# Kernel tuning notes

Hardware: AMD Instinct MI355X
Metric: run time of the kernel (lower is better)

The kernel has to match this reference:

```python
import jax, jax.numpy as jnp
import numpy as np

N_HEADS = 8
DIM = 128
BT, A, M = 2880, 10, 350  # bs*T, agents, map tokens (from forwards())
TOPK_SELF, TOPK_CROSS = 3, 32


def _split_heads(x, h):
    B, T, C = x.shape
    return x.reshape(B, T, h, C // h).transpose(0, 2, 1, 3)  # [B,h,T,hd]


def _biased_attn(q, k, v, pe, rel):
    """flex_attention with score_mod: score + pe[b,q,rel[b,q,kv],h], -inf where rel==-1.
    q:[B,H,Tq,d] k,v:[B,H,Tk,d] pe:[B,Tq,K,H] rel:[B,Tq,Tk] int"""
    d = q.shape[-1]
    scores = jnp.einsum('bhqd,bhkd->bhqk', q, k) / jnp.sqrt(jnp.asarray(d, q.dtype))
    safe = jnp.maximum(rel, 0)
    bias = jnp.take_along_axis(pe, safe[:, :, :, None], axis=2)  # [B,Tq,Tk,H]
    bias = bias.transpose(0, 3, 1, 2)                            # [B,H,Tq,Tk]
    scores = jnp.where(rel[:, None, :, :] > -1, scores + bias, -jnp.inf)
    attn = jax.nn.softmax(scores, axis=-1)
    out = jnp.einsum('bhqk,bhkd->bhqd', attn, v)
    B, H, Tq, hd = out.shape
    return out.transpose(0, 2, 1, 3).reshape(B, Tq, H * hd)


def _make_relation(key, B, Tq, Tk, topk):
    # topk random keys per query get offsets 0..topk-1 in ascending kv order; rest -1
    rand = jax.random.uniform(key, (B, Tq, Tk))
    idx = jnp.sort(jax.lax.top_k(rand, topk)[1], axis=-1)  # [B,Tq,topk]
    rel = jnp.full((B, Tq, Tk), -1, dtype=jnp.int32)
    b = jnp.arange(B)[:, None, None]
    qi = jnp.arange(Tq)[None, :, None]
    return rel.at[b, qi, idx].set(jnp.arange(topk, dtype=jnp.int32)[None, None, :])


def setup_inputs() -> dict:
    key = jax.random.key(0)
    ks = jax.random.split(key, 12)
    s = 0.02
    return {
        'a_token': jax.random.normal(ks[0], (BT, A, DIM), jnp.float32),
        'm_token': jax.random.normal(ks[1], (BT, M, DIM), jnp.float32),
        'a2m_pe': jax.random.uniform(ks[2], (BT, A, TOPK_CROSS, N_HEADS), jnp.float32),
        'a_pe': jax.random.uniform(ks[3], (BT, A, TOPK_SELF, N_HEADS), jnp.float32),
        'Wq': s * jax.random.normal(ks[4], (DIM, DIM), jnp.float32),
        'Wk': s * jax.random.normal(ks[5], (DIM, DIM), jnp.float32),
        'Wv': s * jax.random.normal(ks[6], (DIM, DIM), jnp.float32),
        'W_cross_proj': s * jax.random.normal(ks[7], (DIM, DIM), jnp.float32),
        'W_cattn': s * jax.random.normal(ks[8], (DIM, 3 * DIM), jnp.float32),
        'W_self_proj': s * jax.random.normal(ks[9], (DIM, DIM), jnp.float32),
        'a2m_relation': _make_relation(ks[10], BT, A, M, TOPK_CROSS),
        'a_relation': _make_relation(ks[11], BT, A, A, TOPK_SELF),
    }


def reference(a_token, m_token, a2m_pe, a_pe, Wq, Wk, Wv, W_cross_proj,
              W_cattn, W_self_proj, a2m_relation, a_relation):
    # cross attention: q from a_token, k/v from m_token (dropout=0 => identity)
    q = _split_heads(a_token @ Wq, N_HEADS)
    k = _split_heads(m_token @ Wk, N_HEADS)
    v = _split_heads(m_token @ Wv, N_HEADS)
    y = _biased_attn(q, k, v, a2m_pe, a2m_relation) @ W_cross_proj
    # self attention with fused qkv projection
    q2, k2, v2 = jnp.split(y @ W_cattn, 3, axis=-1)
    y2 = _biased_attn(_split_heads(q2, N_HEADS), _split_heads(k2, N_HEADS),
                      _split_heads(v2, N_HEADS), a_pe, a_relation)
    return y2 @ W_self_proj
```

## Files before the change

### kernel.cpp

```cpp
#include <hip/hip_runtime.h>
#include <hip/hip_bf16.h>


typedef __attribute__((ext_vector_type(4))) float f32x4;
typedef __attribute__((ext_vector_type(8))) short bf16x8v;
typedef __attribute__((ext_vector_type(4))) short short4v;

#define BT_N 2880
#define A_N  10
#define M_N  350
#define BQ_N (BT_N * A_N)
#define DIMC 128

static __device__ __forceinline__ short f2b(float x) {
    __hip_bfloat16 b = __float2bfloat16(x);
    return __builtin_bit_cast(short, b);
}
static __device__ __forceinline__ float b2f(short s) {
    unsigned u = ((unsigned)(unsigned short)s) << 16;
    return __builtin_bit_cast(float, u);
}

__global__ __launch_bounds__(256) void precompute_mats(
    const float* __restrict__ Wq, const float* __restrict__ Wk,
    const float* __restrict__ Wv, const float* __restrict__ Wcp,
    const float* __restrict__ Wc, const float* __restrict__ Wsp,
    short* __restrict__ S1t, short* __restrict__ VP1t,
    short* __restrict__ S2t, short* __restrict__ VP2t)
{
    int gid = blockIdx.x * 256 + threadIdx.x;
    int mat = gid >> 17;
    int idx = gid & 131071;
    float acc = 0.f;
    if (mat == 0) {
        int n = idx >> 7, c = idx & 127;
        int h = n >> 7, d = n & 127;
        #pragma unroll
        for (int t = 0; t < 16; ++t)
            acc += Wq[c * 128 + h * 16 + t] * Wk[d * 128 + h * 16 + t];
        S1t[idx] = f2b(acc * 0.25f);
    } else if (mat == 1) {
        int d = idx >> 10, o = idx & 1023;
        int h = o >> 7, c = o & 127;
        #pragma unroll
        for (int t = 0; t < 16; ++t)
            acc += Wv[c * 128 + h * 16 + t] * Wcp[(h * 16 + t) * 128 + d];
        VP1t[idx] = f2b(acc);
    } else if (mat == 2) {
        int n = idx >> 7, c = idx & 127;
        int h = n >> 7, d = n & 127;
        #pragma unroll
        for (int t = 0; t < 16; ++t)
            acc += Wc[c * 384 + h * 16 + t] * Wc[d * 384 + 128 + h * 16 + t];
        S2t[idx] = f2b(acc * 0.25f);
    } else {
        int d = idx >> 10, o = idx & 1023;
        int h = o >> 7, c = o & 127;
        #pragma unroll
        for (int t = 0; t < 16; ++t)
            acc += Wc[c * 384 + 256 + h * 16 + t] * Wsp[(h * 16 + t) * 128 + d];
        VP2t[idx] = f2b(acc);
    }
}

__global__ __launch_bounds__(256) void conv_bf16(
    const float* __restrict__ in, short* __restrict__ out)
{
    int i = blockIdx.x * 256 + threadIdx.x;
    f32x4 a = ((const f32x4*)in)[2 * i];
    f32x4 b = ((const f32x4*)in)[2 * i + 1];
    bf16x8v t;
    t[0] = f2b(a.x); t[1] = f2b(a.y); t[2] = f2b(a.z); t[3] = f2b(a.w);
    t[4] = f2b(b.x); t[5] = f2b(b.y); t[6] = f2b(b.z); t[7] = f2b(b.w);
    ((bf16x8v*)out)[i] = t;
}

template<bool CF32>
__global__ __launch_bounds__(256) void gemm_bt(
    const short* __restrict__ Ap, const short* __restrict__ Bt,
    void* __restrict__ Cp, int M, int N, int K)
{
    __shared__ short As[128][72];
    __shared__ short Bs[128][72];
    const int tid  = threadIdx.x;
    const int bm   = blockIdx.y << 7, bn = blockIdx.x << 7;
    const int wave = tid >> 6, lane = tid & 63;
    const int wm   = (wave >> 1) << 6, wn = (wave & 1) << 6;
    const int row16 = lane & 15, kq = (lane >> 4) << 3;
    f32x4 acc[4][4] = {};

    for (int k0 = 0; k0 < K; k0 += 64) {
        #pragma unroll
        for (int i = 0; i < 4; ++i) {
            int g = (i << 8) + tid;
            int r = g >> 3, c = (g & 7) << 3;
            *(bf16x8v*)&As[r][c] = *(const bf16x8v*)(Ap + (size_t)(bm + r) * K + k0 + c);
        }
        #pragma unroll
        for (int i = 0; i < 4; ++i) {
            int g = (i << 8) + tid;
            int r = g >> 3, c = (g & 7) << 3;
            *(bf16x8v*)&Bs[r][c] = *(const bf16x8v*)(Bt + (size_t)(bn + r) * K + k0 + c);
        }
        __syncthreads();
        #pragma unroll
        for (int kk = 0; kk < 64; kk += 32) {
            bf16x8v afr[4], bfr[4];
            #pragma unroll
            for (int mi = 0; mi < 4; ++mi)
                afr[mi] = *(const bf16x8v*)&As[wm + (mi << 4) + row16][kq + kk];
            #pragma unroll
            for (int ni = 0; ni < 4; ++ni)
                bfr[ni] = *(const bf16x8v*)&Bs[wn + (ni << 4) + row16][kq + kk];
            #pragma unroll
            for (int mi = 0; mi < 4; ++mi)
                #pragma unroll
                for (int ni = 0; ni < 4; ++ni)
                    acc[mi][ni] = __builtin_amdgcn_mfma_f32_16x16x32_bf16(
                        afr[mi], bfr[ni], acc[mi][ni], 0, 0, 0);
        }
        __syncthreads();
    }

    const int col = lane & 15, rb = (lane >> 4) << 2;
    #pragma unroll
    for (int mi = 0; mi < 4; ++mi)
        #pragma unroll
        for (int ni = 0; ni < 4; ++ni)
            #pragma unroll
            for (int r = 0; r < 4; ++r) {
                int rr = bm + wm + (mi << 4) + rb + r;
                int cc = bn + wn + (ni << 4) + col;
                float v = acc[mi][ni][r];
                if (CF32) ((float*)Cp)[(size_t)rr * N + cc] = v;
                else      ((short*)Cp)[(size_t)rr * N + cc] = f2b(v);
            }
}

__global__ __launch_bounds__(256) void attn_cross(
    const float* __restrict__ m_token, const short* __restrict__ qS,
    const float* __restrict__ pe, const int* __restrict__ rel,
    short* __restrict__ u)
{
    __shared__ short mrows[32][136];
    __shared__ short qsr[16][136];
    __shared__ float sc[32][17];
    __shared__ float wts[8][33];
    __shared__ float peL[256];
    __shared__ int   selk[32];

    const int phys = blockIdx.x;
    const int b    = (phys & 7) * 360 + (phys >> 3) / A_N;
    const int q    = (phys >> 3) % A_N;
    const int bq   = b * A_N + q;
    const int tid  = threadIdx.x;
    const int wave = tid >> 6, lane = tid & 63;
    const int row16 = lane & 15, kq8 = (lane >> 4) << 3;

    const int* relrow = rel + (size_t)bq * M_N;
    for (int k = tid; k < M_N; k += 256) {
        int r = relrow[k];
        if (r >= 0) selk[r] = k;
    }
    if (tid < 128) {
        int h = tid >> 4, c8 = (tid & 15) << 3;
        *(bf16x8v*)&qsr[h][c8] = *(const bf16x8v*)(qS + (size_t)bq * 1024 + h * 128 + c8);
    }
    for (int g = tid; g < 1088; g += 256) ((short*)qsr)[1088 + g] = 0;
    peL[tid] = pe[(size_t)bq * 256 + tid];
    __syncthreads();

    {
        int r = tid >> 3, c16 = (tid & 7) << 4;
        const float* src = m_token + ((size_t)b * M_N + selk[r]) * DIMC + c16;
        f32x4 v0 = *(const f32x4*)(src);
        f32x4 v1 = *(const f32x4*)(src + 4);
        f32x4 v2 = *(const f32x4*)(src + 8);
        f32x4 v3 = *(const f32x4*)(src + 12);
        bf16x8v t0, t1;
        t0[0] = f2b(v0.x); t0[1] = f2b(v0.y); t0[2] = f2b(v0.z); t0[3] = f2b(v0.w);
        t0[4] = f2b(v1.x); t0[5] = f2b(v1.y); t0[6] = f2b(v1.z); t0[7] = f2b(v1.w);
        t1[0] = f2b(v2.x); t1[1] = f2b(v2.y); t1[2] = f2b(v2.z); t1[3] = f2b(v2.w);
        t1[4] = f2b(v3.x); t1[5] = f2b(v3.y); t1[6] = f2b(v3.z); t1[7] = f2b(v3.w);
        *(bf16x8v*)&mrows[r][c16]     = t0;
        *(bf16x8v*)&mrows[r][c16 + 8] = t1;
    }
    __syncthreads();

    if (wave < 2) {
        f32x4 acc = {0.f, 0.f, 0.f, 0.f};
        #pragma unroll
        for (int kc = 0; kc < 4; ++kc) {
            bf16x8v a  = *(const bf16x8v*)&mrows[(wave << 4) + row16][(kc << 5) + kq8];
            bf16x8v bb = *(const bf16x8v*)&qsr[row16][(kc << 5) + kq8];
            acc = __builtin_amdgcn_mfma_f32_16x16x32_bf16(a, bb, acc, 0, 0, 0);
        }
        const int rb4 = (lane >> 4) << 2;
        #pragma unroll
        for (int r = 0; r < 4; ++r)
            sc[(wave << 4) + rb4 + r][row16] = acc[r];
    }
    __syncthreads();

    {
        const int h = tid >> 5, r = tid & 31;
        float s = sc[r][h] + peL[r * 8 + h];
        float mx = s;
        #pragma unroll
        for (int off = 16; off; off >>= 1) mx = fmaxf(mx, __shfl_xor(mx, off, 32));
        float e = __expf(s - mx);
        float su = e;
        #pragma unroll
        for (int off = 16; off; off >>= 1) su += __shfl_xor(su, off, 32);
        wts[h][r] = e / su;
    }
    __syncthreads();

    {
        const int h = tid >> 5, d0 = (tid << 2) & 127;
        f32x4 acc = {0.f, 0.f, 0.f, 0.f};
        #pragma unroll
        for (int r = 0; r < 32; ++r) {
            float w = wts[h][r];
            short4v mv = *(const short4v*)&mrows[r][d0];
            acc.x += w * b2f(mv.x);
            acc.y += w * b2f(mv.y);
            acc.z += w * b2f(mv.z);
            acc.w += w * b2f(mv.w);
        }
        short4v t;
        t.x = f2b(acc.x); t.y = f2b(acc.y); t.z = f2b(acc.z); t.w = f2b(acc.w);
        *(short4v*)(u + (size_t)bq * 1024 + (tid << 2)) = t;
    }
}

__global__ __launch_bounds__(256) void attn_self(
    const short* __restrict__ ybf, const short* __restrict__ yS2,
    const float* __restrict__ pe, const int* __restrict__ rel,
    short* __restrict__ u2)
{
    __shared__ float yrows[3][132];
    __shared__ float ysr[1024];
    __shared__ int   selk[3];
    __shared__ float sw[8][3];
    const int bq = blockIdx.x;
    const int b  = bq / A_N;
    const int tid = threadIdx.x;

    if (tid < A_N) {
        int r = rel[(size_t)bq * A_N + tid];
        if (r >= 0) selk[r] = tid;
    }
    {
        short4v v = ((const short4v*)(yS2 + (size_t)bq * 1024))[tid];
        ysr[(tid << 2) + 0] = b2f(v.x);
        ysr[(tid << 2) + 1] = b2f(v.y);
        ysr[(tid << 2) + 2] = b2f(v.z);
        ysr[(tid << 2) + 3] = b2f(v.w);
    }
    __syncthreads();
    if (tid < 48) {
        int r = tid >> 4, c = (tid & 15) << 3;
        bf16x8v v = *(const bf16x8v*)(ybf + ((size_t)b * A_N + selk[r]) * DIMC + c);
        #pragma unroll
        for (int j = 0; j < 8; ++j) yrows[r][c + j] = b2f(v[j]);
    }
    __syncthreads();
    if (tid < 24) {
        int h = tid / 3, r = tid - h * 3;
        const float* qh = ysr + (h << 7);
        f32x4 p = {0.f, 0.f, 0.f, 0.f};
        #pragma unroll
        for (int d = 0; d < DIMC; d += 4)
            p += *(const f32x4*)(qh + d) * *(const f32x4*)&yrows[r][d];
        sw[h][r] = p.x + p.y + p.z + p.w + pe[((size_t)bq * 3 + r) * 8 + h];
    }
    __syncthreads();
    if (tid < 8) {
        float s0 = sw[tid][0], s1 = sw[tid][1], s2 = sw[tid][2];
        float mx = fmaxf(s0, fmaxf(s1, s2));
        float e0 = __expf(s0 - mx), e1 = __expf(s1 - mx), e2 = __expf(s2 - mx);
        float inv = 1.f / (e0 + e1 + e2);
        sw[tid][0] = e0 * inv; sw[tid][1] = e1 * inv; sw[tid][2] = e2 * inv;
    }
    __syncthreads();
    {
        const int h = tid >> 5, d0 = (tid << 2) & 127;
        f32x4 acc = sw[h][0] * *(const f32x4*)&yrows[0][d0]
                  + sw[h][1] * *(const f32x4*)&yrows[1][d0]
                  + sw[h][2] * *(const f32x4*)&yrows[2][d0];
        short4v t;
        t.x = f2b(acc.x); t.y = f2b(acc.y); t.z = f2b(acc.z); t.w = f2b(acc.w);
        *(short4v*)(u2 + (size_t)bq * 1024 + (tid << 2)) = t;
    }
}

extern "C" void kernel_launch(void* const* d_in, const int* in_sizes, int n_in,
                              void* d_out, int out_size, void* d_ws, size_t ws_size,
                              hipStream_t stream)
{
    const float* a_token = (const float*)d_in[0];
    const float* m_token = (const float*)d_in[1];
    const float* a2m_pe  = (const float*)d_in[2];
    const float* a_pe    = (const float*)d_in[3];
    const float* Wq      = (const float*)d_in[4];
    const float* Wk      = (const float*)d_in[5];
    const float* Wv      = (const float*)d_in[6];
    const float* Wcp     = (const float*)d_in[7];
    const float* Wc      = (const float*)d_in[8];
    const float* Wsp     = (const float*)d_in[9];
    const int*   a2m_rel = (const int*)d_in[10];
    const int*   a_rel   = (const int*)d_in[11];

    char* ws = (char*)d_ws;
    short* S1t  = (short*)(ws + 0);
    short* VP1t = (short*)(ws + 262144);
    short* S2t  = (short*)(ws + 524288);
    short* VP2t = (short*)(ws + 786432);
    short* buf1 = (short*)(ws + 1048576);
    short* buf2 = (short*)(ws + 1048576 + 58982400ull);
    short* ybf  = (short*)(ws + 1048576 + 2ull * 58982400ull);
    short* abf  = (short*)(ws + 1048576 + 2ull * 58982400ull + 7372800ull);
    float* outp = (float*)d_out;

    precompute_mats<<<dim3(2048), dim3(256), 0, stream>>>(
        Wq, Wk, Wv, Wcp, Wc, Wsp, S1t, VP1t, S2t, VP2t);

    conv_bf16<<<dim3(1800), dim3(256), 0, stream>>>(a_token, abf);

    gemm_bt<false><<<dim3(8, 225), dim3(256), 0, stream>>>(
        abf, S1t, (void*)buf1, BQ_N, 1024, 128);

    attn_cross<<<dim3(BQ_N), dim3(256), 0, stream>>>(
        m_token, buf1, a2m_pe, a2m_rel, buf2);

    gemm_bt<false><<<dim3(1, 225), dim3(256), 0, stream>>>(
        buf2, VP1t, (void*)ybf, BQ_N, 128, 1024);

    gemm_bt<false><<<dim3(8, 225), dim3(256), 0, stream>>>(
        ybf, S2t, (void*)buf1, BQ_N, 1024, 128);

    attn_self<<<dim3(BQ_N), dim3(256), 0, stream>>>(
        ybf, buf1, a_pe, a_rel, buf2);

    gemm_bt<true><<<dim3(1, 225), dim3(256), 0, stream>>>(
        buf2, VP2t, (void*)outp, BQ_N, 128, 1024);
}
```

Before: 288.2 us.

## Fold cross-output projection into self-attn score GEMM via precomputed combined weight

Precomputes a combined matrix (VP1 composed with S2) so that both ybf (the cross-attention output) and the self-attention query-score tensor come from one K=1024 GEMM over the cross-attention head output. This replaces two sequential GEMMs (a 128-wide projection, then a 1024-wide product over ybf) with a single dual-output GEMM of 9 column tiles. The intent is to drop the dependent launch and the reread of ybf, at the price of a larger K for the score columns and extra bf16 rounding through the composed weight.

Measured after the change: 349.3 us. 21.2% more time.

```diff
diff --git a/kernel.cpp b/kernel.cpp
--- a/kernel.cpp
+++ b/kernel.cpp
@@ -25,8 +25,8 @@
     const float* __restrict__ Wq, const float* __restrict__ Wk,
     const float* __restrict__ Wv, const float* __restrict__ Wcp,
     const float* __restrict__ Wc, const float* __restrict__ Wsp,
-    short* __restrict__ S1t, short* __restrict__ VP1t,
-    short* __restrict__ S2t, short* __restrict__ VP2t)
+    short* __restrict__ S1t, short* __restrict__ B2t ,
+    short* __restrict__ VP1n, short* __restrict__ S2t, short* __restrict__ VP2t)
 {
     int gid = blockIdx.x * 256 + threadIdx.x;
     int mat = gid >> 17;
@@ -45,7 +45,9 @@
         #pragma unroll
         for (int t = 0; t < 16; ++t)
             acc += Wv[c * 128 + h * 16 + t] * Wcp[(h * 16 + t) * 128 + d];
-        VP1t[idx] = f2b(acc);
+        short v = f2b(acc);
+        B2t[idx] = v;
+        VP1n[o * 128 + d] = v;
     } else if (mat == 2) {
         int n = idx >> 7, c = idx & 127;
         int h = n >> 7, d = n & 127;
@@ -134,6 +136,67 @@
                 float v = acc[mi][ni][r];
                 if (CF32) ((float*)Cp)[(size_t)rr * N + cc] = v;
                 else      ((short*)Cp)[(size_t)rr * N + cc] = f2b(v);
+            }
+}
+
+__global__ __launch_bounds__(256) void gemm_dual(
+    const short* __restrict__ Ap, const short* __restrict__ Bt,
+    short* __restrict__ Cy, short* __restrict__ Cs, int M, int K)
+{
+    __shared__ short As[128][72];
+    __shared__ short Bs[128][72];
+    const int tid  = threadIdx.x;
+    const int bm   = blockIdx.y << 7, bn = blockIdx.x << 7;
+    const int wave = tid >> 6, lane = tid & 63;
+    const int wm   = (wave >> 1) << 6, wn = (wave & 1) << 6;
+    const int row16 = lane & 15, kq = (lane >> 4) << 3;
+    f32x4 acc[4][4] = {};
+
+    for (int k0 = 0; k0 < K; k0 += 64) {
+        #pragma unroll
+        for (int i = 0; i < 4; ++i) {
+            int g = (i << 8) + tid;
+            int r = g >> 3, c = (g & 7) << 3;
+            *(bf16x8v*)&As[r][c] = *(const bf16x8v*)(Ap + (size_t)(bm + r) * K + k0 + c);
+        }
+        #pragma unroll
+        for (int i = 0; i < 4; ++i) {
+            int g = (i << 8) + tid;
+            int r = g >> 3, c = (g & 7) << 3;
+            *(bf16x8v*)&Bs[r][c] = *(const bf16x8v*)(Bt + (size_t)(bn + r) * K + k0 + c);
+        }
+        __syncthreads();
+        #pragma unroll
+        for (int kk = 0; kk < 64; kk += 32) {
+            bf16x8v afr[4], bfr[4];
+            #pragma unroll
+            for (int mi = 0; mi < 4; ++mi)
+                afr[mi] = *(const bf16x8v*)&As[wm + (mi << 4) + row16][kq + kk];
+            #pragma unroll
+            for (int ni = 0; ni < 4; ++ni)
+                bfr[ni] = *(const bf16x8v*)&Bs[wn + (ni << 4) + row16][kq + kk];
+            #pragma unroll
+            for (int mi = 0; mi < 4; ++mi)
+                #pragma unroll
+                for (int ni = 0; ni < 4; ++ni)
+                    acc[mi][ni] = __builtin_amdgcn_mfma_f32_16x16x32_bf16(
+                        afr[mi], bfr[ni], acc[mi][ni], 0, 0, 0);
+        }
+        __syncthreads();
+    }
+
+    const int col = lane & 15, rb = (lane >> 4) << 2;
+    #pragma unroll
+    for (int mi = 0; mi < 4; ++mi)
+        #pragma unroll
+        for (int ni = 0; ni < 4; ++ni)
+            #pragma unroll
+            for (int r = 0; r < 4; ++r) {
+                int rr = bm + wm + (mi << 4) + rb + r;
+                int cl = wn + (ni << 4) + col;
+                short v = f2b(acc[mi][ni][r]);
+                if (bn == 0) Cy[(size_t)rr * 128 + cl] = v;
+                else         Cs[(size_t)rr * 1024 + (bn - 128) + cl] = v;
             }
 }
 
@@ -314,17 +377,21 @@
 
     char* ws = (char*)d_ws;
     short* S1t  = (short*)(ws + 0);
-    short* VP1t = (short*)(ws + 262144);
+    short* VP1n = (short*)(ws + 262144);
     short* S2t  = (short*)(ws + 524288);
     short* VP2t = (short*)(ws + 786432);
     short* buf1 = (short*)(ws + 1048576);
     short* buf2 = (short*)(ws + 1048576 + 58982400ull);
     short* ybf  = (short*)(ws + 1048576 + 2ull * 58982400ull);
     short* abf  = (short*)(ws + 1048576 + 2ull * 58982400ull + 7372800ull);
+    short* B2t  = (short*)(ws + 133758976ull);
     float* outp = (float*)d_out;
 
     precompute_mats<<<dim3(2048), dim3(256), 0, stream>>>(
-        Wq, Wk, Wv, Wcp, Wc, Wsp, S1t, VP1t, S2t, VP2t);
+        Wq, Wk, Wv, Wcp, Wc, Wsp, S1t, B2t, VP1n, S2t, VP2t);
+
+    gemm_bt<false><<<dim3(8, 8), dim3(256), 0, stream>>>(
+        S2t, VP1n, (void*)(B2t + 131072), 1024, 1024, 128);
 
     conv_bf16<<<dim3(1800), dim3(256), 0, stream>>>(a_token, abf);
 
@@ -334,11 +401,8 @@
     attn_cross<<<dim3(BQ_N), dim3(256), 0, stream>>>(
         m_token, buf1, a2m_pe, a2m_rel, buf2);
 
-    gemm_bt<false><<<dim3(1, 225), dim3(256), 0, stream>>>(
-        buf2, VP1t, (void*)ybf, BQ_N, 128, 1024);
-
-    gemm_bt<false><<<dim3(8, 225), dim3(256), 0, stream>>>(
-        ybf, S2t, (void*)buf1, BQ_N, 1024, 128);
+    gemm_dual<<<dim3(9, 225), dim3(256), 0, stream>>>(
+        buf2, B2t, ybf, buf1, BQ_N, 1024);
 
     attn_self<<<dim3(BQ_N), dim3(256), 0, stream>>>(
         ybf, buf1, a_pe, a_rel, buf2);
```
